# Kernel tuning notes

Hardware: AMD Instinct MI355X
Metric: run time of the kernel (lower is better)

The kernel has to match this reference:

```python
import jax, jax.numpy as jnp
import numpy as np

N_SUBJECTS = 16
N_LABELS = 8
DENS_TEMP = 0.1  # args.ProtoSim_dens_temp


def setup_inputs() -> dict:
    key = jax.random.key(0)
    k1, k2, k3 = jax.random.split(key, 3)
    B, V, D = 131072, 2, 128
    X_data = jax.random.normal(k1, (B, V, D), dtype=jnp.float32)
    subject = jax.random.randint(k2, (B,), 0, N_SUBJECTS, dtype=jnp.int64) if jax.config.read('jax_enable_x64') else jax.random.randint(k2, (B,), 0, N_SUBJECTS)
    labels = jax.random.randint(k3, (B,), 0, N_LABELS)
    return {"X_data": X_data, "subject": subject, "labels": labels}


def reference(X_data, subject, labels):
    B, V, D = X_data.shape
    G = N_SUBJECTS * N_LABELS
    # torch.cat(torch.unbind(X_data, dim=1), dim=0): view-major ordering -> [V*B, D]
    cf = jnp.transpose(X_data, (1, 0, 2)).reshape(V * B, D)
    # subject/labels duplicated once (module assumes 2 views)
    seg = jnp.tile(subject * N_LABELS + labels, V)  # group id per row, [V*B]
    counts = jax.ops.segment_sum(jnp.ones((V * B,), jnp.float32), seg, num_segments=G)
    centroid = jax.ops.segment_sum(cf, seg, num_segments=G) / counts[:, None]  # [G, D]
    # per-point euclidean distance to own group centroid (torch.cdist to 1-row centroid)
    dist = jnp.linalg.norm(cf - centroid[seg], axis=1)  # [V*B]
    # density: mean(sqrt(dist)) / log(n + 10) for groups with n > 1, else 0 then dmax
    dens = (jax.ops.segment_sum(jnp.sqrt(dist), seg, num_segments=G) / counts) / jnp.log(counts + 10.0)
    dens = jnp.where(counts > 1, dens, 0.0)
    dens = jnp.where(counts > 1, dens, dens.max())
    lo = jnp.percentile(dens, 10.0)
    hi = jnp.percentile(dens, 90.0)
    dens = jnp.clip(dens, lo, hi)
    dens = DENS_TEMP * dens / dens.mean()
    cen_of_cen = centroid.mean(axis=0)  # [D]
    sim = jnp.exp((centroid @ cen_of_cen) / dens)  # [G]
    sim = sim - sim.max()
    return -sim.mean()
```

## Files before the change

### kernel.cpp

```cpp
#include <hip/hip_runtime.h>
#include <cstdint>
#include <cstddef>

#define BPTS    131072
#define D_DIM   128
#define G_GR    128
#define NL      8
#define NSLC    16
#define PERMBUF 128
#define NBLK_S  64
#define PPB     (BPTS / NBLK_S)

__global__ __launch_bounds__(256) void k_hist(const int* __restrict__ sub,
                                              const int* __restrict__ lab,
                                              int* __restrict__ hblk) {
    __shared__ int h[G_GR];
    int t = threadIdx.x, blk = blockIdx.x;
    if (t < G_GR) h[t] = 0;
    __syncthreads();
    int b0 = blk * PPB;
    for (int i = t; i < PPB; i += 256)
        atomicAdd(&h[sub[b0 + i] * NL + lab[b0 + i]], 1);
    __syncthreads();
    if (t < G_GR) hblk[blk * G_GR + t] = h[t];
}

__global__ __launch_bounds__(256) void k_scatter(const int* __restrict__ sub,
                                                 const int* __restrict__ lab,
                                                 const int* __restrict__ hblk,
                                                 int* __restrict__ counts,
                                                 int* __restrict__ offsets,
                                                 float* __restrict__ countsf,
                                                 int* __restrict__ perm) {
    __shared__ int tot[G_GR];
    __shared__ int cur[G_GR];
    int t = threadIdx.x, blk = blockIdx.x;
    if (t < G_GR) {
        int tt = 0, mine = 0;
        for (int b = 0; b < NBLK_S; ++b) {
            int v = hblk[b * G_GR + t];
            tt += v;
            if (b < blk) mine += v;
        }
        tot[t] = tt;
        cur[t] = mine;
    }
    __syncthreads();
    if (t < G_GR) {
        int off = 0;
        for (int j = 0; j < t; ++j) off += tot[j];
        cur[t] += off;
        if (blk == 0) {
            counts[t]  = tot[t];
            offsets[t] = off;
            countsf[t] = 2.0f * (float)tot[t];
        }
    }
    __syncthreads();
    int b0 = blk * PPB;
    for (int i = t; i < PPB; i += 256) {
        int p = b0 + i;
        int g = sub[p] * NL + lab[p];
        int s = atomicAdd(&cur[g], 1);
        perm[s] = p;
    }
}

__global__ __launch_bounds__(256) void k_psum(const float4* __restrict__ X4,
                                              const int* __restrict__ perm,
                                              const int* __restrict__ offsets,
                                              const int* __restrict__ counts,
                                              float* __restrict__ part) {
    __shared__ int   pbuf[PERMBUF];
    __shared__ float red[4 * 256];
    int g = blockIdx.x >> 4, s = blockIdx.x & 15;
    int off = offsets[g], len = counts[g];
    int lo = off + (len * s) / NSLC;
    int hi = off + (len * (s + 1)) / NSLC;
    int slen = hi - lo;
    int t = threadIdx.x, lane = t & 63, w = t >> 6;

    for (int j = t; j < slen; j += 256) pbuf[j] = perm[lo + j];
    __syncthreads();

    float4 acc = make_float4(0.f, 0.f, 0.f, 0.f);
    for (int i = w * 8; i < slen; i += 32) {
        int idx[8];
#pragma unroll
        for (int u = 0; u < 8; ++u) {
            int j = i + u;
            idx[u] = pbuf[(j < slen) ? j : (slen - 1)];
        }
        float4 x[8];
#pragma unroll
        for (int u = 0; u < 8; ++u) x[u] = X4[(size_t)idx[u] * 64 + lane];
#pragma unroll
        for (int u = 0; u < 8; ++u) {
            if (i + u < slen) {
                acc.x += x[u].x; acc.y += x[u].y;
                acc.z += x[u].z; acc.w += x[u].w;
            }
        }
    }
    red[w * 256 + lane * 4 + 0] = acc.x;
    red[w * 256 + lane * 4 + 1] = acc.y;
    red[w * 256 + lane * 4 + 2] = acc.z;
    red[w * 256 + lane * 4 + 3] = acc.w;
    __syncthreads();
    if (t < 128) {
        float v = 0.f;
        for (int r = 0; r < 4; ++r)
            v += red[r * 256 + t] + red[r * 256 + t + 128];
        part[(size_t)blockIdx.x * 128 + t] = v;
    }
}

__global__ __launch_bounds__(256) void k_dist(const float4* __restrict__ X4,
                                              const int* __restrict__ perm,
                                              const int* __restrict__ offsets,
                                              const int* __restrict__ counts,
                                              const float* __restrict__ part,
                                              float* __restrict__ centroid,
                                              float* __restrict__ dpart) {
    __shared__ int   pbuf[PERMBUF];
    __shared__ float cen[D_DIM];
    __shared__ float wsum[4];
    int g = blockIdx.x >> 4, s = blockIdx.x & 15;
    int off = offsets[g], len = counts[g];
    int lo = off + (len * s) / NSLC;
    int hi = off + (len * (s + 1)) / NSLC;
    int slen = hi - lo;
    int t = threadIdx.x, lane = t & 63, w = t >> 6;

    if (t < D_DIM) {
        float v = 0.f;
        for (int s2 = 0; s2 < NSLC; ++s2)
            v += part[(size_t)(g * NSLC + s2) * 128 + t];
        float c = (len > 0) ? v / (2.0f * (float)len) : 0.f;
        cen[t] = c;
        if (s == 0) centroid[g * D_DIM + t] = c;
    }
    for (int j = t; j < slen; j += 256) pbuf[j] = perm[lo + j];
    __syncthreads();

    int cd = (lane & 31) * 4;
    float4 c = make_float4(cen[cd], cen[cd + 1], cen[cd + 2], cen[cd + 3]);

    float sacc = 0.f;
    for (int i = w * 8; i < slen; i += 32) {
        int idx[8];
#pragma unroll
        for (int u = 0; u < 8; ++u) {
            int j = i + u;
            idx[u] = pbuf[(j < slen) ? j : (slen - 1)];
        }
        float4 x[8];
#pragma unroll
        for (int u = 0; u < 8; ++u) x[u] = X4[(size_t)idx[u] * 64 + lane];
#pragma unroll
        for (int u = 0; u < 8; ++u) {
            float dx = x[u].x - c.x, dy = x[u].y - c.y;
            float dz = x[u].z - c.z, dw = x[u].w - c.w;
            float d = dx * dx + dy * dy + dz * dz + dw * dw;
#pragma unroll
            for (int m = 1; m <= 16; m <<= 1) d += __shfl_xor(d, m);
            if (i + u < slen) sacc += sqrtf(sqrtf(d));
        }
    }
    float t2 = sacc + __shfl_xor(sacc, 32);
    if (lane == 0) wsum[w] = t2;
    __syncthreads();
    if (t == 0) dpart[blockIdx.x] = wsum[0] + wsum[1] + wsum[2] + wsum[3];
}

__global__ __launch_bounds__(128) void k_final(const float* __restrict__ dpart,
                                               const float* __restrict__ countsf,
                                               const float* __restrict__ centroid,
                                               float* __restrict__ out) {
    __shared__ float srt[G_GR];
    __shared__ float red[G_GR];
    __shared__ float coc[D_DIM];
    int t = threadIdx.x;

    float ds = 0.f;
    for (int s = 0; s < NSLC; ++s) ds += dpart[t * NSLC + s];
    float cnt  = countsf[t];
    float dens = (cnt > 1.f) ? (ds / cnt) / logf(cnt + 10.f) : 0.f;

    red[t] = dens;
    __syncthreads();
    for (int s = 64; s > 0; s >>= 1) {
        if (t < s) red[t] = fmaxf(red[t], red[t + s]);
        __syncthreads();
    }
    float dmax = red[0];
    __syncthreads();
    if (!(cnt > 1.f)) dens = dmax;

    srt[t] = dens;
    __syncthreads();
    for (int k = 2; k <= G_GR; k <<= 1) {
        for (int j = k >> 1; j > 0; j >>= 1) {
            int ixj = t ^ j;
            if (ixj > t) {
                float a = srt[t], b = srt[ixj];
                bool up = ((t & k) == 0);
                if ((a > b) == up) { srt[t] = b; srt[ixj] = a; }
            }
            __syncthreads();
        }
    }
    double p10 = 0.10 * 127.0, p90 = 0.90 * 127.0;
    int   i10 = (int)p10,           i90 = (int)p90;
    float f10 = (float)(p10 - i10), f90 = (float)(p90 - i90);
    float lo = srt[i10] + f10 * (srt[i10 + 1] - srt[i10]);
    float hi = srt[i90] + f90 * (srt[i90 + 1] - srt[i90]);
    dens = fminf(fmaxf(dens, lo), hi);

    red[t] = dens;
    __syncthreads();
    for (int s = 64; s > 0; s >>= 1) {
        if (t < s) red[t] += red[t + s];
        __syncthreads();
    }
    float dmean = red[0] / 128.f;
    __syncthreads();
    dens = 0.1f * dens / dmean;

    float cs = 0.f;
    for (int g = 0; g < G_GR; ++g) cs += centroid[g * D_DIM + t];
    coc[t] = cs / 128.f;
    __syncthreads();

    float dot = 0.f;
    for (int d = 0; d < D_DIM; ++d) dot += centroid[t * D_DIM + d] * coc[d];
    float sim = expf(dot / dens);

    red[t] = sim;
    __syncthreads();
    for (int s = 64; s > 0; s >>= 1) {
        if (t < s) red[t] = fmaxf(red[t], red[t + s]);
        __syncthreads();
    }
    float smax = red[0];
    __syncthreads();
    red[t] = sim - smax;
    __syncthreads();
    for (int s = 64; s > 0; s >>= 1) {
        if (t < s) red[t] += red[t + s];
        __syncthreads();
    }
    if (t == 0) out[0] = -(red[0] / 128.f);
}

extern "C" void kernel_launch(void* const* d_in, const int* in_sizes, int n_in,
                              void* d_out, int out_size, void* d_ws, size_t ws_size,
                              hipStream_t stream) {
    const float4* X4      = (const float4*)d_in[0];
    const int*    subject = (const int*)d_in[1];
    const int*    labels  = (const int*)d_in[2];
    float*        out     = (float*)d_out;
    char*         ws      = (char*)d_ws;

    size_t o = 0;
    int*   hblk     = (int*)(ws + o);   o += (size_t)NBLK_S * G_GR * 4;
    int*   counts   = (int*)(ws + o);   o += 512;
    int*   offsets  = (int*)(ws + o);   o += 512;
    float* countsf  = (float*)(ws + o); o += 512;
    int*   perm     = (int*)(ws + o);   o += (size_t)BPTS * 4;
    float* part     = (float*)(ws + o); o += (size_t)G_GR * NSLC * 128 * 4;
    float* centroid = (float*)(ws + o); o += (size_t)G_GR * D_DIM * 4;
    float* dpart    = (float*)(ws + o); o += (size_t)G_GR * NSLC * 4;

    k_hist   <<<NBLK_S, 256, 0, stream>>>(subject, labels, hblk);
    k_scatter<<<NBLK_S, 256, 0, stream>>>(subject, labels, hblk, counts, offsets, countsf, perm);
    k_psum   <<<G_GR * NSLC, 256, 0, stream>>>(X4, perm, offsets, counts, part);
    k_dist   <<<G_GR * NSLC, 256, 0, stream>>>(X4, perm, offsets, counts, part, centroid, dpart);
    k_final  <<<1, 128, 0, stream>>>(dpart, countsf, centroid, out);
}
```

Before: 242.8 us.

## Locally sort scatter writes in shared memory and deepen gather unroll to 16

The scatter kernel now counting-sorts each block's points by group in shared memory before writing, so the global perm writes come out as contiguous runs per group instead of being scattered by atomics. This aims to improve write coalescing. Separately, the centroid-sum and distance kernels load 16 rows per wave per iteration instead of 8, keeping more gather loads in flight at the cost of more registers per thread.

New measurement: 256.5 us. 1.06x slower.

```diff
diff --git a/kernel.cpp b/kernel.cpp
--- a/kernel.cpp
+++ b/kernel.cpp
@@ -32,37 +32,65 @@
                                                  int* __restrict__ offsets,
                                                  float* __restrict__ countsf,
                                                  int* __restrict__ perm) {
-    __shared__ int tot[G_GR];
-    __shared__ int cur[G_GR];
+    __shared__ int lcnt[G_GR];
+    __shared__ int loff[G_GR];
+    __shared__ int gbase[G_GR];
+    __shared__ int ids[PPB];
+    __shared__ int gslot[PPB];
     int t = threadIdx.x, blk = blockIdx.x;
+
+    if (t < G_GR) lcnt[t] = 0;
+    __syncthreads();
+
+    int b0 = blk * PPB;
+    int garr[PPB / 256], carr[PPB / 256];
+#pragma unroll
+    for (int r = 0; r < PPB / 256; ++r) {
+        int i = b0 + r * 256 + t;
+        int g = sub[i] * NL + lab[i];
+        garr[r] = g;
+        carr[r] = atomicAdd(&lcnt[g], 1);
+    }
+    __syncthreads();
+
     if (t < G_GR) {
+        int o = 0;
+        for (int j = 0; j < t; ++j) o += lcnt[j];
+        loff[t] = o;
         int tt = 0, mine = 0;
         for (int b = 0; b < NBLK_S; ++b) {
             int v = hblk[b * G_GR + t];
             tt += v;
             if (b < blk) mine += v;
         }
-        tot[t] = tt;
-        cur[t] = mine;
+        if (blk == 0) {
+            counts[t]  = tt;
+            countsf[t] = 2.0f * (float)tt;
+        }
+        gbase[t] = tt;
     }
     __syncthreads();
     if (t < G_GR) {
         int off = 0;
-        for (int j = 0; j < t; ++j) off += tot[j];
-        cur[t] += off;
-        if (blk == 0) {
-            counts[t]  = tot[t];
-            offsets[t] = off;
-            countsf[t] = 2.0f * (float)tot[t];
-        }
-    }
-    __syncthreads();
-    int b0 = blk * PPB;
-    for (int i = t; i < PPB; i += 256) {
-        int p = b0 + i;
-        int g = sub[p] * NL + lab[p];
-        int s = atomicAdd(&cur[g], 1);
-        perm[s] = p;
+        for (int j = 0; j < t; ++j) off += gbase[j];
+        if (blk == 0) offsets[t] = off;
+        int mine = 0;
+        for (int b = 0; b < blk; ++b) mine += hblk[b * G_GR + t];
+        gbase[t] = off + mine;
+    }
+    __syncthreads();
+
+#pragma unroll
+    for (int r = 0; r < PPB / 256; ++r) {
+        int slot = loff[garr[r]] + carr[r];
+        ids[slot]   = b0 + r * 256 + t;
+        gslot[slot] = garr[r];
+    }
+    __syncthreads();
+
+    for (int j = t; j < PPB; j += 256) {
+        int g = gslot[j];
+        perm[gbase[g] + (j - loff[g])] = ids[j];
     }
 }
 
@@ -84,19 +112,19 @@
     __syncthreads();
 
     float4 acc = make_float4(0.f, 0.f, 0.f, 0.f);
-    for (int i = w * 8; i < slen; i += 32) {
-        int idx[8];
-#pragma unroll
-        for (int u = 0; u < 8; ++u) {
-            int j = i + u;
+    for (int base = w * 16; base < slen; base += 64) {
+        int idx[16];
+#pragma unroll
+        for (int u = 0; u < 16; ++u) {
+            int j = base + u;
             idx[u] = pbuf[(j < slen) ? j : (slen - 1)];
         }
-        float4 x[8];
-#pragma unroll
-        for (int u = 0; u < 8; ++u) x[u] = X4[(size_t)idx[u] * 64 + lane];
-#pragma unroll
-        for (int u = 0; u < 8; ++u) {
-            if (i + u < slen) {
+        float4 x[16];
+#pragma unroll
+        for (int u = 0; u < 16; ++u) x[u] = X4[(size_t)idx[u] * 64 + lane];
+#pragma unroll
+        for (int u = 0; u < 16; ++u) {
+            if (base + u < slen) {
                 acc.x += x[u].x; acc.y += x[u].y;
                 acc.z += x[u].z; acc.w += x[u].w;
             }
@@ -147,24 +175,24 @@
     float4 c = make_float4(cen[cd], cen[cd + 1], cen[cd + 2], cen[cd + 3]);
 
     float sacc = 0.f;
-    for (int i = w * 8; i < slen; i += 32) {
-        int idx[8];
-#pragma unroll
-        for (int u = 0; u < 8; ++u) {
-            int j = i + u;
+    for (int base = w * 16; base < slen; base += 64) {
+        int idx[16];
+#pragma unroll
+        for (int u = 0; u < 16; ++u) {
+            int j = base + u;
             idx[u] = pbuf[(j < slen) ? j : (slen - 1)];
         }
-        float4 x[8];
-#pragma unroll
-        for (int u = 0; u < 8; ++u) x[u] = X4[(size_t)idx[u] * 64 + lane];
-#pragma unroll
-        for (int u = 0; u < 8; ++u) {
+        float4 x[16];
+#pragma unroll
+        for (int u = 0; u < 16; ++u) x[u] = X4[(size_t)idx[u] * 64 + lane];
+#pragma unroll
+        for (int u = 0; u < 16; ++u) {
             float dx = x[u].x - c.x, dy = x[u].y - c.y;
             float dz = x[u].z - c.z, dw = x[u].w - c.w;
             float d = dx * dx + dy * dy + dz * dz + dw * dw;
 #pragma unroll
             for (int m = 1; m <= 16; m <<= 1) d += __shfl_xor(d, m);
-            if (i + u < slen) sacc += sqrtf(sqrtf(d));
+            if (base + u < slen) sacc += sqrtf(sqrtf(d));
         }
     }
     float t2 = sacc + __shfl_xor(sacc, 32);
```

## Replace sort-by-group permutation with per-slice filtering and streaming distance pass

Applied to the files above, without the earlier changes.

Drops the histogram and scatter kernels that built a group-sorted permutation. The partial-sum kernel now has each (group, slice) block scan a contiguous range of points and collect matching indices into shared memory. A small reduce kernel then forms the centroids. The distance pass streams points in their original order, looks up each point's centroid from a shared-memory copy of all centroids, and accumulates per-group sums with shared atomics. The intent is to remove two launches and the scattered gathers in the distance pass, at the cost of every psum block rereading the full label arrays (128× redundant label traffic) and a larger final reduction.

New measurement: 256.5 us. +5.6%, slower.

```diff
diff --git a/kernel.cpp b/kernel.cpp
--- a/kernel.cpp
+++ b/kernel.cpp
@@ -2,101 +2,54 @@
 #include <cstdint>
 #include <cstddef>
 
-#define BPTS    131072
-#define D_DIM   128
-#define G_GR    128
-#define NL      8
-#define NSLC    16
-#define PERMBUF 128
-#define NBLK_S  64
-#define PPB     (BPTS / NBLK_S)
-
-__global__ __launch_bounds__(256) void k_hist(const int* __restrict__ sub,
+#define BPTS   131072
+#define D_DIM  128
+#define G_GR   128
+#define NL     8
+#define NSLC   32
+#define RANGE  (BPTS / NSLC)
+#define DBLK   512
+#define DPTS   (BPTS / DBLK)
+
+__global__ __launch_bounds__(256) void k_psum(const float4* __restrict__ X4,
+                                              const int* __restrict__ sub,
                                               const int* __restrict__ lab,
-                                              int* __restrict__ hblk) {
-    __shared__ int h[G_GR];
-    int t = threadIdx.x, blk = blockIdx.x;
-    if (t < G_GR) h[t] = 0;
-    __syncthreads();
-    int b0 = blk * PPB;
-    for (int i = t; i < PPB; i += 256)
-        atomicAdd(&h[sub[b0 + i] * NL + lab[b0 + i]], 1);
-    __syncthreads();
-    if (t < G_GR) hblk[blk * G_GR + t] = h[t];
-}
-
-__global__ __launch_bounds__(256) void k_scatter(const int* __restrict__ sub,
-                                                 const int* __restrict__ lab,
-                                                 const int* __restrict__ hblk,
-                                                 int* __restrict__ counts,
-                                                 int* __restrict__ offsets,
-                                                 float* __restrict__ countsf,
-                                                 int* __restrict__ perm) {
-    __shared__ int tot[G_GR];
-    __shared__ int cur[G_GR];
-    int t = threadIdx.x, blk = blockIdx.x;
-    if (t < G_GR) {
-        int tt = 0, mine = 0;
-        for (int b = 0; b < NBLK_S; ++b) {
-            int v = hblk[b * G_GR + t];
-            tt += v;
-            if (b < blk) mine += v;
-        }
-        tot[t] = tt;
-        cur[t] = mine;
-    }
-    __syncthreads();
-    if (t < G_GR) {
-        int off = 0;
-        for (int j = 0; j < t; ++j) off += tot[j];
-        cur[t] += off;
-        if (blk == 0) {
-            counts[t]  = tot[t];
-            offsets[t] = off;
-            countsf[t] = 2.0f * (float)tot[t];
-        }
-    }
-    __syncthreads();
-    int b0 = blk * PPB;
-    for (int i = t; i < PPB; i += 256) {
-        int p = b0 + i;
-        int g = sub[p] * NL + lab[p];
-        int s = atomicAdd(&cur[g], 1);
-        perm[s] = p;
-    }
-}
-
-__global__ __launch_bounds__(256) void k_psum(const float4* __restrict__ X4,
-                                              const int* __restrict__ perm,
-                                              const int* __restrict__ offsets,
-                                              const int* __restrict__ counts,
-                                              float* __restrict__ part) {
-    __shared__ int   pbuf[PERMBUF];
+                                              float* __restrict__ part,
+                                              int* __restrict__ cnt) {
+    __shared__ int   list[RANGE];
+    __shared__ int   nm;
     __shared__ float red[4 * 256];
-    int g = blockIdx.x >> 4, s = blockIdx.x & 15;
-    int off = offsets[g], len = counts[g];
-    int lo = off + (len * s) / NSLC;
-    int hi = off + (len * (s + 1)) / NSLC;
-    int slen = hi - lo;
+    int g = blockIdx.x >> 5, s = blockIdx.x & 31;
     int t = threadIdx.x, lane = t & 63, w = t >> 6;
 
-    for (int j = t; j < slen; j += 256) pbuf[j] = perm[lo + j];
-    __syncthreads();
+    if (t == 0) nm = 0;
+    __syncthreads();
+
+    int p0 = s * RANGE;
+    for (int i = t; i < RANGE; i += 256) {
+        int p = p0 + i;
+        if (sub[p] * NL + lab[p] == g) {
+            int k = atomicAdd(&nm, 1);
+            list[k] = p;
+        }
+    }
+    __syncthreads();
+    int n = nm;
 
     float4 acc = make_float4(0.f, 0.f, 0.f, 0.f);
-    for (int i = w * 8; i < slen; i += 32) {
+    for (int i = w * 8; i < n; i += 32) {
         int idx[8];
 #pragma unroll
         for (int u = 0; u < 8; ++u) {
             int j = i + u;
-            idx[u] = pbuf[(j < slen) ? j : (slen - 1)];
+            idx[u] = list[(j < n) ? j : (n - 1)];
         }
         float4 x[8];
 #pragma unroll
         for (int u = 0; u < 8; ++u) x[u] = X4[(size_t)idx[u] * 64 + lane];
 #pragma unroll
         for (int u = 0; u < 8; ++u) {
-            if (i + u < slen) {
+            if (i + u < n) {
                 acc.x += x[u].x; acc.y += x[u].y;
                 acc.z += x[u].z; acc.w += x[u].w;
             }
@@ -113,64 +66,68 @@
             v += red[r * 256 + t] + red[r * 256 + t + 128];
         part[(size_t)blockIdx.x * 128 + t] = v;
     }
-}
-
-__global__ __launch_bounds__(256) void k_dist(const float4* __restrict__ X4,
-                                              const int* __restrict__ perm,
-                                              const int* __restrict__ offsets,
-                                              const int* __restrict__ counts,
-                                              const float* __restrict__ part,
-                                              float* __restrict__ centroid,
+    if (t == 0) cnt[blockIdx.x] = n;
+}
+
+__global__ __launch_bounds__(256) void k_reduce(const float* __restrict__ part,
+                                                const int* __restrict__ cnt,
+                                                float* __restrict__ centroid,
+                                                float* __restrict__ countsf) {
+    int i = blockIdx.x * 256 + threadIdx.x;
+    if (i >= G_GR * D_DIM) return;
+    int g = i >> 7, d = i & 127;
+    float v = 0.f;
+    int   n = 0;
+    for (int s = 0; s < NSLC; ++s) {
+        v += part[(size_t)(g * NSLC + s) * 128 + d];
+        n += cnt[g * NSLC + s];
+    }
+    centroid[i] = (n > 0) ? v / (2.0f * (float)n) : 0.f;
+    if (d == 0) countsf[g] = 2.0f * (float)n;
+}
+
+__global__ __launch_bounds__(512) void k_dist(const float4* __restrict__ X4,
+                                              const int* __restrict__ sub,
+                                              const int* __restrict__ lab,
+                                              const float* __restrict__ centroid,
                                               float* __restrict__ dpart) {
-    __shared__ int   pbuf[PERMBUF];
-    __shared__ float cen[D_DIM];
-    __shared__ float wsum[4];
-    int g = blockIdx.x >> 4, s = blockIdx.x & 15;
-    int off = offsets[g], len = counts[g];
-    int lo = off + (len * s) / NSLC;
-    int hi = off + (len * (s + 1)) / NSLC;
-    int slen = hi - lo;
+    __shared__ float4 cen4[G_GR * 32];
+    __shared__ float  dsum[G_GR];
     int t = threadIdx.x, lane = t & 63, w = t >> 6;
 
-    if (t < D_DIM) {
-        float v = 0.f;
-        for (int s2 = 0; s2 < NSLC; ++s2)
-            v += part[(size_t)(g * NSLC + s2) * 128 + t];
-        float c = (len > 0) ? v / (2.0f * (float)len) : 0.f;
-        cen[t] = c;
-        if (s == 0) centroid[g * D_DIM + t] = c;
-    }
-    for (int j = t; j < slen; j += 256) pbuf[j] = perm[lo + j];
-    __syncthreads();
-
-    int cd = (lane & 31) * 4;
-    float4 c = make_float4(cen[cd], cen[cd + 1], cen[cd + 2], cen[cd + 3]);
-
-    float sacc = 0.f;
-    for (int i = w * 8; i < slen; i += 32) {
-        int idx[8];
-#pragma unroll
-        for (int u = 0; u < 8; ++u) {
-            int j = i + u;
-            idx[u] = pbuf[(j < slen) ? j : (slen - 1)];
+    const float4* c4 = (const float4*)centroid;
+    for (int i = t; i < G_GR * 32; i += 512) cen4[i] = c4[i];
+    if (t < G_GR) dsum[t] = 0.f;
+    __syncthreads();
+
+    int p0 = blockIdx.x * DPTS;
+    int q  = lane & 31;
+    for (int i = w * 8; i < DPTS; i += 64) {
+        int pg[8];
+#pragma unroll
+        for (int u = 0; u < 8; ++u) {
+            int p = p0 + i + u;
+            pg[u] = sub[p] * NL + lab[p];
         }
         float4 x[8];
 #pragma unroll
-        for (int u = 0; u < 8; ++u) x[u] = X4[(size_t)idx[u] * 64 + lane];
-#pragma unroll
-        for (int u = 0; u < 8; ++u) {
+        for (int u = 0; u < 8; ++u)
+            x[u] = X4[(size_t)(p0 + i + u) * 64 + lane];
+#pragma unroll
+        for (int u = 0; u < 8; ++u) {
+            float4 c = cen4[pg[u] * 32 + q];
             float dx = x[u].x - c.x, dy = x[u].y - c.y;
             float dz = x[u].z - c.z, dw = x[u].w - c.w;
             float d = dx * dx + dy * dy + dz * dz + dw * dw;
 #pragma unroll
             for (int m = 1; m <= 16; m <<= 1) d += __shfl_xor(d, m);
-            if (i + u < slen) sacc += sqrtf(sqrtf(d));
-        }
-    }
-    float t2 = sacc + __shfl_xor(sacc, 32);
-    if (lane == 0) wsum[w] = t2;
-    __syncthreads();
-    if (t == 0) dpart[blockIdx.x] = wsum[0] + wsum[1] + wsum[2] + wsum[3];
+            float sd = sqrtf(sqrtf(d));
+            float tot = sd + __shfl_down(sd, 32);
+            if (lane == 0) atomicAdd(&dsum[pg[u]], tot);
+        }
+    }
+    __syncthreads();
+    if (t < G_GR) dpart[(size_t)blockIdx.x * G_GR + t] = dsum[t];
 }
 
 __global__ __launch_bounds__(128) void k_final(const float* __restrict__ dpart,
@@ -183,7 +140,7 @@
     int t = threadIdx.x;
 
     float ds = 0.f;
-    for (int s = 0; s < NSLC; ++s) ds += dpart[t * NSLC + s];
+    for (int b = 0; b < DBLK; ++b) ds += dpart[(size_t)b * G_GR + t];
     float cnt  = countsf[t];
     float dens = (cnt > 1.f) ? (ds / cnt) / logf(cnt + 10.f) : 0.f;
 
@@ -263,18 +220,14 @@
     char*         ws      = (char*)d_ws;
 
     size_t o = 0;
-    int*   hblk     = (int*)(ws + o);   o += (size_t)NBLK_S * G_GR * 4;
-    int*   counts   = (int*)(ws + o);   o += 512;
-    int*   offsets  = (int*)(ws + o);   o += 512;
+    float* part     = (float*)(ws + o); o += (size_t)G_GR * NSLC * 128 * 4;
+    int*   cnt      = (int*)(ws + o);   o += (size_t)G_GR * NSLC * 4;
+    float* centroid = (float*)(ws + o); o += (size_t)G_GR * D_DIM * 4;
     float* countsf  = (float*)(ws + o); o += 512;
-    int*   perm     = (int*)(ws + o);   o += (size_t)BPTS * 4;
-    float* part     = (float*)(ws + o); o += (size_t)G_GR * NSLC * 128 * 4;
-    float* centroid = (float*)(ws + o); o += (size_t)G_GR * D_DIM * 4;
-    float* dpart    = (float*)(ws + o); o += (size_t)G_GR * NSLC * 4;
-
-    k_hist   <<<NBLK_S, 256, 0, stream>>>(subject, labels, hblk);
-    k_scatter<<<NBLK_S, 256, 0, stream>>>(subject, labels, hblk, counts, offsets, countsf, perm);
-    k_psum   <<<G_GR * NSLC, 256, 0, stream>>>(X4, perm, offsets, counts, part);
-    k_dist   <<<G_GR * NSLC, 256, 0, stream>>>(X4, perm, offsets, counts, part, centroid, dpart);
-    k_final  <<<1, 128, 0, stream>>>(dpart, countsf, centroid, out);
-}
+    float* dpart    = (float*)(ws + o); o += (size_t)DBLK * G_GR * 4;
+
+    k_psum  <<<G_GR * NSLC, 256, 0, stream>>>(X4, subject, labels, part, cnt);
+    k_reduce<<<(G_GR * D_DIM + 255) / 256, 256, 0, stream>>>(part, cnt, centroid, countsf);
+    k_dist  <<<DBLK, 512, 0, stream>>>(X4, subject, labels, centroid, dpart);
+    k_final <<<1, 128, 0, stream>>>(dpart, countsf, centroid, out);
+}
```
